# Performance work log

Measured on AMD Instinct MI355X. Metric: run time of the kernel, lower is better.

Reference implementation:

```python
import jax, jax.numpy as jnp
import numpy as np

N = 50000   # nodes
E = 800000  # edges
G = 64      # graphs in batch
EPS = 1e-5  # BatchNorm eps


def setup_inputs() -> dict:
    key = jax.random.key(0)
    ks = jax.random.split(key, 32)
    inp = {
        'x': jax.random.normal(ks[0], (N, 1), jnp.float32),
        'edge_index': jax.random.randint(ks[1], (2, E), 0, N),
        'batch': jnp.sort(jax.random.randint(ks[2], (N,), 0, G)),
    }
    dims = [(1, 64), (64, 64), (64, 64), (64, 64)]
    for i, (din, dout) in enumerate(dims, 1):
        inp[f'W{i}'] = jax.random.normal(ks[2 + i], (din, dout), jnp.float32) / np.sqrt(din)
        inp[f'b{i}'] = jnp.zeros((dout,), jnp.float32)
        inp[f'g{i}'] = jnp.ones((dout,), jnp.float32)
        inp[f'bt{i}'] = jnp.zeros((dout,), jnp.float32)
    inp['fw1'] = jax.random.normal(ks[10], (128, 64), jnp.float32) / 8.0
    inp['fb1'] = jnp.zeros((128,), jnp.float32)
    inp['fw2'] = jax.random.normal(ks[11], (10, 128), jnp.float32) / np.sqrt(128)
    inp['fb2'] = jnp.zeros((10,), jnp.float32)
    return inp


def _gcn_norm(edge_index):
    # add self-loops, symmetric normalization (PyG GCNConv default)
    loop = jnp.arange(N)
    row = jnp.concatenate([edge_index[0], loop])
    col = jnp.concatenate([edge_index[1], loop])
    deg = jax.ops.segment_sum(jnp.ones_like(col, jnp.float32), col, num_segments=N)
    dinv = jnp.where(deg > 0, deg ** -0.5, 0.0)
    norm = dinv[row] * dinv[col]
    return row, col, norm


def _gcn(x, W, b, row, col, norm):
    h = x @ W                                   # [N, dout]
    msg = h[row] * norm[:, None]                # gather + scale per edge
    agg = jax.ops.segment_sum(msg, col, num_segments=N)  # scatter-add
    return agg + b


def _bn(x, g, bt):
    m = x.mean(0)
    v = x.var(0)
    return g * (x - m) * jax.lax.rsqrt(v + EPS) + bt


def reference(x, edge_index, batch,
              W1, b1, g1, bt1, W2, b2, g2, bt2,
              W3, b3, g3, bt3, W4, b4, g4, bt4,
              fw1, fb1, fw2, fb2):
    row, col, norm = _gcn_norm(edge_index)
    x = jax.nn.relu(_bn(_gcn(x, W1, b1, row, col, norm), g1, bt1))
    x = jax.nn.relu(_bn(_gcn(x, W2, b2, row, col, norm), g2, bt2))
    x = jax.nn.relu(_bn(_gcn(x, W3, b3, row, col, norm), g3, bt3))
    x = jax.nn.relu(_bn(_gcn(x, W4, b4, row, col, norm), g4, bt4))
    # global mean pool over graphs
    cnt = jax.ops.segment_sum(jnp.ones((N,), jnp.float32), batch, num_segments=G)
    pooled = jax.ops.segment_sum(x, batch, num_segments=G) / jnp.clip(cnt, 1.0)[:, None]
    h = jax.nn.relu(pooled @ fw1.T + fb1)
    return h @ fw2.T + fb2
```

## Files before the change

### kernel.cpp

```cpp
#include <hip/hip_runtime.h>

#define NN 50000
#define NE 800000
#define NG 64
#define FD 64
#define BN_EPS 1e-5f
#define SCAN_B 256
#define SCAN_NBLK ((NN + SCAN_B - 1) / SCAN_B)
#define NBIN 98
#define BINCAP 12288
#define SCH 4096
#define SCH_NBLK ((NE + SCH - 1) / SCH)

__global__ __launch_bounds__(256) void k_binscatter(const int* __restrict__ row,
                                                    const int* __restrict__ col,
                                                    int* __restrict__ gcnt,
                                                    int* __restrict__ bins) {
    __shared__ int stage[SCH];
    __shared__ int cnt[NBIN], off[NBIN + 1], cur[NBIN], gbase[NBIN];
    int t = threadIdx.x;
    int e0 = blockIdx.x * SCH;
    int nk = NE - e0; if (nk > SCH) nk = SCH;
    if (nk <= 0) return;
    for (int b = t; b < NBIN; b += 256) cnt[b] = 0;
    __syncthreads();
    for (int k = t; k < nk; k += 256) {
        int c = col[e0 + k];
        atomicAdd(&cnt[c >> 9], 1);
    }
    __syncthreads();
    if (t == 0) {
        int run = 0;
        for (int b = 0; b < NBIN; ++b) { off[b] = run; run += cnt[b]; }
        off[NBIN] = run;
    }
    __syncthreads();
    if (t < NBIN) {
        cur[t] = off[t];
        gbase[t] = t * BINCAP + atomicAdd(&gcnt[t], cnt[t]);
    }
    __syncthreads();
    for (int k = t; k < nk; k += 256) {
        int c = col[e0 + k];
        int r = row[e0 + k];
        int b = c >> 9;
        int pos = atomicAdd(&cur[b], 1);
        stage[pos] = ((c & 511) << 16) | r;
    }
    __syncthreads();
    for (int k = t; k < nk; k += 256) {
        int lo = 0, hi = NBIN - 1;
        while (lo < hi) {
            int mid = (lo + hi + 1) >> 1;
            if (off[mid] <= k) lo = mid; else hi = mid - 1;
        }
        bins[gbase[lo] + (k - off[lo])] = stage[k];
    }
}

__global__ __launch_bounds__(256) void k_bindeg(const int* __restrict__ gcnt,
                                                const int* __restrict__ bins,
                                                int* __restrict__ deg) {
    __shared__ int ldeg[512];
    int b = blockIdx.x, t = threadIdx.x;
    for (int l = t; l < 512; l += 256) ldeg[l] = 0;
    __syncthreads();
    int nb = gcnt[b];
    const int* bp = bins + b * BINCAP;
    for (int k = t; k < nb; k += 256) atomicAdd(&ldeg[bp[k] >> 16], 1);
    __syncthreads();
    int base = b << 9;
    for (int l = t; l < 512; l += 256) {
        int i = base + l;
        if (i < NN) deg[i] = ldeg[l];
    }
}

__global__ __launch_bounds__(SCAN_B) void k_scan_blk(const int* __restrict__ deg,
                                                     int* __restrict__ cursor,
                                                     int* __restrict__ bsum,
                                                     float* __restrict__ dinv) {
    __shared__ int sh[SCAN_B];
    int b = blockIdx.x, t = threadIdx.x;
    int i = b * SCAN_B + t;
    int v = (i < NN) ? deg[i] : 0;
    if (i < NN) dinv[i] = rsqrtf((float)v + 1.0f);
    sh[t] = v;
    __syncthreads();
    for (int off = 1; off < SCAN_B; off <<= 1) {
        int u = (t >= off) ? sh[t - off] : 0;
        __syncthreads();
        sh[t] += u;
        __syncthreads();
    }
    if (i < NN) cursor[i] = sh[t] - v;
    if (t == SCAN_B - 1) bsum[b] = sh[t];
}

__global__ __launch_bounds__(SCAN_B) void k_scan_top(int* __restrict__ bsum) {
    __shared__ int sh[SCAN_B];
    int t = threadIdx.x;
    int v = (t < SCAN_NBLK) ? bsum[t] : 0;
    sh[t] = v;
    __syncthreads();
    for (int off = 1; off < SCAN_B; off <<= 1) {
        int u = (t >= off) ? sh[t - off] : 0;
        __syncthreads();
        sh[t] += u;
        __syncthreads();
    }
    if (t < SCAN_NBLK) bsum[t] = sh[t] - v;
}

__global__ __launch_bounds__(SCAN_B) void k_scan_add(int* __restrict__ cursor,
                                                     const int* __restrict__ bsum) {
    int b = blockIdx.x, t = threadIdx.x;
    int i = b * SCAN_B + t;
    if (i < NN) cursor[i] += bsum[b];
}

__global__ __launch_bounds__(256) void k_binfill(const int* __restrict__ gcnt,
                                                 const int* __restrict__ bins,
                                                 const int* __restrict__ cursor,
                                                 int* __restrict__ eidx) {
    __shared__ int lcur[512];
    int b = blockIdx.x, t = threadIdx.x;
    int base = b << 9;
    for (int l = t; l < 512; l += 256) {
        int i = base + l;
        lcur[l] = (i < NN) ? cursor[i] : 0;
    }
    __syncthreads();
    int nb = gcnt[b];
    const int* bp = bins + b * BINCAP;
    for (int k = t; k < nb; k += 256) {
        int v = bp[k];
        int pos = atomicAdd(&lcur[v >> 16], 1);
        eidx[pos] = v & 0xFFFF;
    }
}

__global__ void k_xd(const float* __restrict__ x, const float* __restrict__ dinv,
                     float* __restrict__ xd) {
    int i = blockIdx.x * blockDim.x + threadIdx.x;
    if (i < NN) xd[i] = x[i] * dinv[i];
}

__global__ void k_l1_gather(const int* __restrict__ cursor, const int* __restrict__ eidx,
                            const float* __restrict__ xd, const float* __restrict__ x,
                            const float* __restrict__ dinv, float* __restrict__ s) {
    int i = blockIdx.x * blockDim.x + threadIdx.x;
    if (i < NN) {
        int start = cursor[i];
        int end = (i < NN - 1) ? cursor[i + 1] : NE;
        float acc = 0.0f;
        for (int k = start; k < end; ++k) acc += xd[eidx[k]];
        float di = dinv[i];
        s[i] = di * (acc + di * x[i]);
    }
}

__global__ __launch_bounds__(256) void k_scalar_stats(const float* __restrict__ s,
                                                      float* __restrict__ stats) {
    __shared__ float ls[256], lq[256];
    float a = 0.f, b = 0.f;
    for (int i = blockIdx.x * blockDim.x + threadIdx.x; i < NN; i += gridDim.x * blockDim.x) {
        float v = s[i]; a += v; b += v * v;
    }
    ls[threadIdx.x] = a; lq[threadIdx.x] = b; __syncthreads();
    for (int st = 128; st > 0; st >>= 1) {
        if (threadIdx.x < st) { ls[threadIdx.x] += ls[threadIdx.x + st]; lq[threadIdx.x] += lq[threadIdx.x + st]; }
        __syncthreads();
    }
    if (threadIdx.x == 0) { atomicAdd(&stats[0], ls[0]); atomicAdd(&stats[1], lq[0]); }
}

__global__ void k_l1_coeffs(const float* __restrict__ stats, const float* __restrict__ W1,
                            const float* __restrict__ b1, const float* __restrict__ g1,
                            const float* __restrict__ bt1,
                            float* __restrict__ alpha, float* __restrict__ cshift) {
    int j = threadIdx.x;
    if (j < FD) {
        float mean = stats[0] * (1.0f / NN);
        float var  = stats[1] * (1.0f / NN) - mean * mean;
        float w = W1[j];
        float rinv = rsqrtf(var * w * w + BN_EPS);
        float a = g1[j] * w * rinv;
        alpha[j]  = a;
        cshift[j] = bt1[j] - a * mean;
    }
}

__global__ __launch_bounds__(256) void k_mm_l1(const float* __restrict__ s,
                                               const float* __restrict__ alpha,
                                               const float* __restrict__ cshift,
                                               const float* __restrict__ W,
                                               float* __restrict__ h) {
    __shared__ float Ws[64 * 64];
    __shared__ float xs[4 * 64];
    int t = threadIdx.x;
    for (int k = t; k < 64 * 64; k += 256) Ws[k] = W[k];
    int n0 = blockIdx.x * 4;
    int j = t & 63, n = t >> 6;
    int node = n0 + n;
    float sv = (node < NN) ? s[node] : 0.0f;
    xs[t] = fmaxf(alpha[j] * sv + cshift[j], 0.0f);
    __syncthreads();
    if (node < NN) {
        float acc = 0.f;
        #pragma unroll
        for (int k = 0; k < 64; ++k) acc += xs[n * 64 + k] * Ws[k * 64 + j];
        h[node * 64 + j] = acc;
    }
}

__global__ __launch_bounds__(256) void k_mm_bn(const float* __restrict__ src,
                                               const float* __restrict__ scale,
                                               const float* __restrict__ shift,
                                               const float* __restrict__ W,
                                               float* __restrict__ h) {
    __shared__ float Ws[64 * 64];
    __shared__ float xs[4 * 64];
    int t = threadIdx.x;
    for (int k = t; k < 64 * 64; k += 256) Ws[k] = W[k];
    int n0 = blockIdx.x * 4;
    int j = t & 63, n = t >> 6;
    int node = n0 + n;
    int gidx = n0 * 64 + t;
    float v = (gidx < NN * 64) ? src[gidx] : 0.0f;
    xs[t] = fmaxf(scale[j] * v + shift[j], 0.0f);
    __syncthreads();
    if (node < NN) {
        float acc = 0.f;
        #pragma unroll
        for (int k = 0; k < 64; ++k) acc += xs[n * 64 + k] * Ws[k * 64 + j];
        h[node * 64 + j] = acc;
    }
}

__global__ __launch_bounds__(256) void k_gather(const int* __restrict__ cursor,
                                                const int* __restrict__ eidx,
                                                const float* __restrict__ dinv,
                                                const float* __restrict__ h,
                                                const float* __restrict__ b,
                                                float* __restrict__ agg) {
    int node = blockIdx.x * 4 + (threadIdx.x >> 6);
    if (node >= NN) return;
    int lane = threadIdx.x & 63;
    int eslot = lane >> 4;
    int fb = (lane & 15) << 2;
    int start = cursor[node];
    int end = (node < NN - 1) ? cursor[node + 1] : NE;
    float4 acc = make_float4(0.f, 0.f, 0.f, 0.f);
    for (int e = start + eslot; e < end; e += 4) {
        int r = eidx[e];
        float dr = dinv[r];
        const float4 hv = *reinterpret_cast<const float4*>(&h[r * 64 + fb]);
        acc.x += hv.x * dr; acc.y += hv.y * dr; acc.z += hv.z * dr; acc.w += hv.w * dr;
    }
    acc.x += __shfl_xor(acc.x, 16); acc.y += __shfl_xor(acc.y, 16);
    acc.z += __shfl_xor(acc.z, 16); acc.w += __shfl_xor(acc.w, 16);
    acc.x += __shfl_xor(acc.x, 32); acc.y += __shfl_xor(acc.y, 32);
    acc.z += __shfl_xor(acc.z, 32); acc.w += __shfl_xor(acc.w, 32);
    if (lane < 16) {
        float dc = dinv[node];
        const float4 hv = *reinterpret_cast<const float4*>(&h[node * 64 + fb]);
        const float4 bv = *reinterpret_cast<const float4*>(&b[fb]);
        float4 o;
        o.x = dc * (acc.x + dc * hv.x) + bv.x;
        o.y = dc * (acc.y + dc * hv.y) + bv.y;
        o.z = dc * (acc.z + dc * hv.z) + bv.z;
        o.w = dc * (acc.w + dc * hv.w) + bv.w;
        *reinterpret_cast<float4*>(&agg[node * 64 + fb]) = o;
    }
}

__global__ __launch_bounds__(256) void k_bn_stats(const float* __restrict__ agg,
                                                  float* __restrict__ bnsum, float* __restrict__ bnsq) {
    __shared__ float ls[256], lq[256];
    int j = threadIdx.x & 63, nl = threadIdx.x >> 6;
    float a = 0.f, b = 0.f;
    for (int i = blockIdx.x * 4 + nl; i < NN; i += gridDim.x * 4) {
        float v = agg[i * 64 + j]; a += v; b += v * v;
    }
    ls[threadIdx.x] = a; lq[threadIdx.x] = b; __syncthreads();
    if (threadIdx.x < 128) { ls[threadIdx.x] += ls[threadIdx.x + 128]; lq[threadIdx.x] += lq[threadIdx.x + 128]; }
    __syncthreads();
    if (threadIdx.x < 64) {
        atomicAdd(&bnsum[j], ls[threadIdx.x] + ls[threadIdx.x + 64]);
        atomicAdd(&bnsq[j],  lq[threadIdx.x] + lq[threadIdx.x + 64]);
    }
}

__global__ void k_bn_finalize(const float* __restrict__ bnsum, const float* __restrict__ bnsq,
                              const float* __restrict__ g, const float* __restrict__ bt,
                              float* __restrict__ scale, float* __restrict__ shift) {
    int j = threadIdx.x;
    if (j < FD) {
        float mean = bnsum[j] * (1.0f / NN);
        float var  = bnsq[j] * (1.0f / NN) - mean * mean;
        float rinv = rsqrtf(var + BN_EPS);
        float sc = g[j] * rinv;
        scale[j] = sc;
        shift[j] = bt[j] - sc * mean;
    }
}

__global__ __launch_bounds__(256) void k_pool_bn(const float* __restrict__ agg,
                                                 const float* __restrict__ scale,
                                                 const float* __restrict__ shift,
                                                 const int* __restrict__ batch,
                                                 float* __restrict__ pooled,
                                                 float* __restrict__ cnt) {
    const int wpb = 4;
    int wave = blockIdx.x * wpb + (threadIdx.x >> 6);
    int lane = threadIdx.x & 63;
    const int nwaves = gridDim.x * wpb;
    int chunk = (NN + nwaves - 1) / nwaves;
    int i0 = wave * chunk;
    int i1 = i0 + chunk; if (i1 > NN) i1 = NN;
    if (i0 >= NN) return;
    float sc = scale[lane], sh = shift[lane];
    float acc = 0.0f;
    int curb = batch[i0];
    int runlen = 0;
    for (int i = i0; i < i1; ++i) {
        int b = batch[i];
        if (b != curb) {
            atomicAdd(&pooled[curb * 64 + lane], acc);
            if (lane == 0) atomicAdd(&cnt[curb], (float)runlen);
            acc = 0.0f; runlen = 0; curb = b;
        }
        acc += fmaxf(sc * agg[i * 64 + lane] + sh, 0.0f);
        ++runlen;
    }
    atomicAdd(&pooled[curb * 64 + lane], acc);
    if (lane == 0) atomicAdd(&cnt[curb], (float)runlen);
}

__global__ __launch_bounds__(128) void k_fc(const float* __restrict__ pooled, const float* __restrict__ cnt,
                                            const float* __restrict__ fw1, const float* __restrict__ fb1,
                                            const float* __restrict__ fw2, const float* __restrict__ fb2,
                                            float* __restrict__ out) {
    __shared__ float p[64], hsh[128];
    int g = blockIdx.x, t = threadIdx.x;
    if (t < 64) {
        float c = cnt[g]; c = c < 1.f ? 1.f : c;
        p[t] = pooled[g * 64 + t] / c;
    }
    __syncthreads();
    float acc = fb1[t];
    #pragma unroll 8
    for (int k = 0; k < 64; ++k) acc += p[k] * fw1[t * 64 + k];
    hsh[t] = fmaxf(acc, 0.f);
    __syncthreads();
    if (t < 10) {
        float o = fb2[t];
        #pragma unroll 8
        for (int k = 0; k < 128; ++k) o += hsh[k] * fw2[t * 128 + k];
        out[g * 10 + t] = o;
    }
}

extern "C" void kernel_launch(void* const* d_in, const int* in_sizes, int n_in,
                              void* d_out, int out_size, void* d_ws, size_t ws_size,
                              hipStream_t stream) {
    const float* x   = (const float*)d_in[0];
    const int* ei    = (const int*)d_in[1];
    const int* batch = (const int*)d_in[2];
    const float* W[5]  = {nullptr, (const float*)d_in[3],  (const float*)d_in[7],
                                   (const float*)d_in[11], (const float*)d_in[15]};
    const float* bb[5] = {nullptr, (const float*)d_in[4],  (const float*)d_in[8],
                                   (const float*)d_in[12], (const float*)d_in[16]};
    const float* gg[5] = {nullptr, (const float*)d_in[5],  (const float*)d_in[9],
                                   (const float*)d_in[13], (const float*)d_in[17]};
    const float* bt[5] = {nullptr, (const float*)d_in[6],  (const float*)d_in[10],
                                   (const float*)d_in[14], (const float*)d_in[18]};
    const float* fw1 = (const float*)d_in[19];
    const float* fb1 = (const float*)d_in[20];
    const float* fw2 = (const float*)d_in[21];
    const float* fb2 = (const float*)d_in[22];
    float* out = (float*)d_out;

    const int* row = ei;
    const int* col = ei + NE;

    float* ws = (float*)d_ws;
    int*   cursor  = (int*)ws;
    int*   degi    = (int*)(ws + 50000);
    int*   eidx    = (int*)(ws + 100000);
    float* dinv    = ws + 900000;
    float* xd      = ws + 950000;
    int*   bsum    = (int*)(ws + 1000000);
    float* s       = ws + 1001000;
    float* stats   = ws + 1051008;
    float* bnsum   = ws + 1051072;
    float* bnsq    = ws + 1051136;
    float* scale   = ws + 1051200;
    float* shift   = ws + 1051264;
    float* pooled  = ws + 1051360;
    float* cnt     = ws + 1055456;
    int*   gcnt    = (int*)(ws + 1056000);
    float* hbuf    = ws + 1100000;
    int*   bins    = (int*)(ws + 1100000);
    float* aggbuf  = ws + 4300000;

    const int B = 256;
    int gN  = (NN + B - 1) / B;

    hipMemsetAsync(gcnt, 0, NBIN * sizeof(int), stream);
    k_binscatter<<<SCH_NBLK, B, 0, stream>>>(row, col, gcnt, bins);
    k_bindeg<<<NBIN, B, 0, stream>>>(gcnt, bins, degi);
    k_scan_blk<<<SCAN_NBLK, SCAN_B, 0, stream>>>(degi, cursor, bsum, dinv);
    k_scan_top<<<1, SCAN_B, 0, stream>>>(bsum);
    k_scan_add<<<SCAN_NBLK, SCAN_B, 0, stream>>>(cursor, bsum);
    k_binfill<<<NBIN, B, 0, stream>>>(gcnt, bins, cursor, eidx);

    k_xd<<<gN, B, 0, stream>>>(x, dinv, xd);
    k_l1_gather<<<gN, B, 0, stream>>>(cursor, eidx, xd, x, dinv, s);
    hipMemsetAsync(stats, 0, 2 * sizeof(float), stream);
    k_scalar_stats<<<256, B, 0, stream>>>(s, stats);
    k_l1_coeffs<<<1, 64, 0, stream>>>(stats, W[1], bb[1], gg[1], bt[1], scale, shift);

    k_mm_l1<<<(NN + 3) / 4, B, 0, stream>>>(s, scale, shift, W[2], hbuf);
    k_gather<<<(NN + 3) / 4, B, 0, stream>>>(cursor, eidx, dinv, hbuf, bb[2], aggbuf);
    hipMemsetAsync(bnsum, 0, 128 * sizeof(float), stream);
    k_bn_stats<<<512, B, 0, stream>>>(aggbuf, bnsum, bnsq);
    k_bn_finalize<<<1, 64, 0, stream>>>(bnsum, bnsq, gg[2], bt[2], scale, shift);

    for (int L = 3; L <= 4; ++L) {
        k_mm_bn<<<(NN + 3) / 4, B, 0, stream>>>(aggbuf, scale, shift, W[L], hbuf);
        k_gather<<<(NN + 3) / 4, B, 0, stream>>>(cursor, eidx, dinv, hbuf, bb[L], aggbuf);
        hipMemsetAsync(bnsum, 0, 128 * sizeof(float), stream);
        k_bn_stats<<<512, B, 0, stream>>>(aggbuf, bnsum, bnsq);
        k_bn_finalize<<<1, 64, 0, stream>>>(bnsum, bnsq, gg[L], bt[L], scale, shift);
    }

    hipMemsetAsync(pooled, 0, (64 * 64 + 64) * sizeof(float), stream);
    k_pool_bn<<<512, B, 0, stream>>>(aggbuf, scale, shift, batch, pooled, cnt);
    k_fc<<<NG, 128, 0, stream>>>(pooled, cnt, fw1, fb1, fw2, fb2, out);
}
```

Before: 361.8 us.

## Fuse CSR build, layer-1 stats and BN finalize into neighbouring kernels

Merges degree counting with a per-bin local scan and computes dinv and xd in the same kernel. The global scan-add pass is dropped by applying bin offsets wherever the cursor is read. Layer-1 statistics are reduced inside the gather kernel, and BN scale/shift are recomputed at the start of each consumer kernel instead of in separate finalize kernels. Host memsets become in-kernel zeroing in earlier kernels. The aim is to cut kernel launches and inter-kernel gaps, at the cost of an extra bsum lookup per cursor read and redundant per-block coefficient math.

```diff
diff --git a/kernel.cpp b/kernel.cpp
--- a/kernel.cpp
+++ b/kernel.cpp
@@ -6,11 +6,11 @@
 #define FD 64
 #define BN_EPS 1e-5f
 #define SCAN_B 256
-#define SCAN_NBLK ((NN + SCAN_B - 1) / SCAN_B)
 #define NBIN 98
 #define BINCAP 12288
 #define SCH 4096
 #define SCH_NBLK ((NE + SCH - 1) / SCH)
+#define INV_NN (1.0f / NN)
 
 __global__ __launch_bounds__(256) void k_binscatter(const int* __restrict__ row,
                                                     const int* __restrict__ col,
@@ -58,10 +58,15 @@
     }
 }
 
-__global__ __launch_bounds__(256) void k_bindeg(const int* __restrict__ gcnt,
-                                                const int* __restrict__ bins,
-                                                int* __restrict__ deg) {
+__global__ __launch_bounds__(256) void k_binscan(const int* __restrict__ gcnt,
+                                                 const int* __restrict__ bins,
+                                                 const float* __restrict__ x,
+                                                 int* __restrict__ cursor,
+                                                 int* __restrict__ bsum,
+                                                 float* __restrict__ dinv,
+                                                 float* __restrict__ xd) {
     __shared__ int ldeg[512];
+    __shared__ int psc[256];
     int b = blockIdx.x, t = threadIdx.x;
     for (int l = t; l < 512; l += 256) ldeg[l] = 0;
     __syncthreads();
@@ -69,22 +74,38 @@
     const int* bp = bins + b * BINCAP;
     for (int k = t; k < nb; k += 256) atomicAdd(&ldeg[bp[k] >> 16], 1);
     __syncthreads();
+    int d0 = ldeg[2 * t], d1 = ldeg[2 * t + 1];
+    int pv = d0 + d1;
+    psc[t] = pv;
+    __syncthreads();
+    for (int off = 1; off < 256; off <<= 1) {
+        int u = (t >= off) ? psc[t - off] : 0;
+        __syncthreads();
+        psc[t] += u;
+        __syncthreads();
+    }
+    int excl = psc[t] - pv;
     int base = b << 9;
-    for (int l = t; l < 512; l += 256) {
-        int i = base + l;
-        if (i < NN) deg[i] = ldeg[l];
-    }
-}
-
-__global__ __launch_bounds__(SCAN_B) void k_scan_blk(const int* __restrict__ deg,
-                                                     int* __restrict__ cursor,
-                                                     int* __restrict__ bsum,
-                                                     float* __restrict__ dinv) {
+    int i0 = base + 2 * t, i1 = i0 + 1;
+    if (i0 < NN) {
+        cursor[i0] = excl;
+        float dv = rsqrtf((float)d0 + 1.0f);
+        dinv[i0] = dv; xd[i0] = x[i0] * dv;
+    }
+    if (i1 < NN) {
+        cursor[i1] = excl + d0;
+        float dv = rsqrtf((float)d1 + 1.0f);
+        dinv[i1] = dv; xd[i1] = x[i1] * dv;
+    }
+    if (t == 255) bsum[b] = psc[255];
+}
+
+__global__ __launch_bounds__(SCAN_B) void k_scan_top(int* __restrict__ bsum,
+                                                     float* __restrict__ stats) {
     __shared__ int sh[SCAN_B];
-    int b = blockIdx.x, t = threadIdx.x;
-    int i = b * SCAN_B + t;
-    int v = (i < NN) ? deg[i] : 0;
-    if (i < NN) dinv[i] = rsqrtf((float)v + 1.0f);
+    int t = threadIdx.x;
+    if (t < 2) stats[t] = 0.0f;
+    int v = (t < NBIN) ? bsum[t] : 0;
     sh[t] = v;
     __syncthreads();
     for (int off = 1; off < SCAN_B; off <<= 1) {
@@ -93,42 +114,21 @@
         sh[t] += u;
         __syncthreads();
     }
-    if (i < NN) cursor[i] = sh[t] - v;
-    if (t == SCAN_B - 1) bsum[b] = sh[t];
-}
-
-__global__ __launch_bounds__(SCAN_B) void k_scan_top(int* __restrict__ bsum) {
-    __shared__ int sh[SCAN_B];
-    int t = threadIdx.x;
-    int v = (t < SCAN_NBLK) ? bsum[t] : 0;
-    sh[t] = v;
-    __syncthreads();
-    for (int off = 1; off < SCAN_B; off <<= 1) {
-        int u = (t >= off) ? sh[t - off] : 0;
-        __syncthreads();
-        sh[t] += u;
-        __syncthreads();
-    }
-    if (t < SCAN_NBLK) bsum[t] = sh[t] - v;
-}
-
-__global__ __launch_bounds__(SCAN_B) void k_scan_add(int* __restrict__ cursor,
-                                                     const int* __restrict__ bsum) {
-    int b = blockIdx.x, t = threadIdx.x;
-    int i = b * SCAN_B + t;
-    if (i < NN) cursor[i] += bsum[b];
+    if (t < NBIN) bsum[t] = sh[t] - v;
 }
 
 __global__ __launch_bounds__(256) void k_binfill(const int* __restrict__ gcnt,
                                                  const int* __restrict__ bins,
                                                  const int* __restrict__ cursor,
+                                                 const int* __restrict__ bsum,
                                                  int* __restrict__ eidx) {
     __shared__ int lcur[512];
     int b = blockIdx.x, t = threadIdx.x;
     int base = b << 9;
+    int bofs = bsum[b];
     for (int l = t; l < 512; l += 256) {
         int i = base + l;
-        lcur[l] = (i < NN) ? cursor[i] : 0;
+        lcur[l] = (i < NN) ? cursor[i] + bofs : 0;
     }
     __syncthreads();
     int nb = gcnt[b];
@@ -140,71 +140,63 @@
     }
 }
 
-__global__ void k_xd(const float* __restrict__ x, const float* __restrict__ dinv,
-                     float* __restrict__ xd) {
-    int i = blockIdx.x * blockDim.x + threadIdx.x;
-    if (i < NN) xd[i] = x[i] * dinv[i];
-}
-
-__global__ void k_l1_gather(const int* __restrict__ cursor, const int* __restrict__ eidx,
-                            const float* __restrict__ xd, const float* __restrict__ x,
-                            const float* __restrict__ dinv, float* __restrict__ s) {
-    int i = blockIdx.x * blockDim.x + threadIdx.x;
+__global__ __launch_bounds__(256) void k_l1_gather(const int* __restrict__ cursor,
+                                                   const int* __restrict__ bsum,
+                                                   const int* __restrict__ eidx,
+                                                   const float* __restrict__ xd,
+                                                   const float* __restrict__ x,
+                                                   const float* __restrict__ dinv,
+                                                   float* __restrict__ s,
+                                                   float* __restrict__ stats) {
+    __shared__ float ls[256], lq[256];
+    int t = threadIdx.x;
+    int i = blockIdx.x * 256 + t;
+    float sv = 0.0f;
     if (i < NN) {
-        int start = cursor[i];
-        int end = (i < NN - 1) ? cursor[i + 1] : NE;
+        int start = cursor[i] + bsum[i >> 9];
+        int end = (i < NN - 1) ? cursor[i + 1] + bsum[(i + 1) >> 9] : NE;
         float acc = 0.0f;
         for (int k = start; k < end; ++k) acc += xd[eidx[k]];
         float di = dinv[i];
-        s[i] = di * (acc + di * x[i]);
-    }
-}
-
-__global__ __launch_bounds__(256) void k_scalar_stats(const float* __restrict__ s,
-                                                      float* __restrict__ stats) {
-    __shared__ float ls[256], lq[256];
-    float a = 0.f, b = 0.f;
-    for (int i = blockIdx.x * blockDim.x + threadIdx.x; i < NN; i += gridDim.x * blockDim.x) {
-        float v = s[i]; a += v; b += v * v;
-    }
-    ls[threadIdx.x] = a; lq[threadIdx.x] = b; __syncthreads();
+        sv = di * (acc + di * x[i]);
+        s[i] = sv;
+    }
+    ls[t] = sv; lq[t] = sv * sv;
+    __syncthreads();
     for (int st = 128; st > 0; st >>= 1) {
-        if (threadIdx.x < st) { ls[threadIdx.x] += ls[threadIdx.x + st]; lq[threadIdx.x] += lq[threadIdx.x + st]; }
+        if (t < st) { ls[t] += ls[t + st]; lq[t] += lq[t + st]; }
         __syncthreads();
     }
-    if (threadIdx.x == 0) { atomicAdd(&stats[0], ls[0]); atomicAdd(&stats[1], lq[0]); }
-}
-
-__global__ void k_l1_coeffs(const float* __restrict__ stats, const float* __restrict__ W1,
-                            const float* __restrict__ b1, const float* __restrict__ g1,
-                            const float* __restrict__ bt1,
-                            float* __restrict__ alpha, float* __restrict__ cshift) {
-    int j = threadIdx.x;
-    if (j < FD) {
-        float mean = stats[0] * (1.0f / NN);
-        float var  = stats[1] * (1.0f / NN) - mean * mean;
-        float w = W1[j];
-        float rinv = rsqrtf(var * w * w + BN_EPS);
-        float a = g1[j] * w * rinv;
-        alpha[j]  = a;
-        cshift[j] = bt1[j] - a * mean;
-    }
+    if (t == 0) { atomicAdd(&stats[0], ls[0]); atomicAdd(&stats[1], lq[0]); }
 }
 
 __global__ __launch_bounds__(256) void k_mm_l1(const float* __restrict__ s,
-                                               const float* __restrict__ alpha,
-                                               const float* __restrict__ cshift,
+                                               const float* __restrict__ stats,
+                                               const float* __restrict__ W1,
+                                               const float* __restrict__ g1,
+                                               const float* __restrict__ bt1,
                                                const float* __restrict__ W,
                                                float* __restrict__ h) {
     __shared__ float Ws[64 * 64];
     __shared__ float xs[4 * 64];
+    __shared__ float als[64], cls[64];
     int t = threadIdx.x;
     for (int k = t; k < 64 * 64; k += 256) Ws[k] = W[k];
+    if (t < 64) {
+        float mean = stats[0] * INV_NN;
+        float var  = stats[1] * INV_NN - mean * mean;
+        float w = W1[t];
+        float rinv = rsqrtf(var * w * w + BN_EPS);
+        float a = g1[t] * w * rinv;
+        als[t] = a;
+        cls[t] = bt1[t] - a * mean;
+    }
+    __syncthreads();
     int n0 = blockIdx.x * 4;
     int j = t & 63, n = t >> 6;
     int node = n0 + n;
     float sv = (node < NN) ? s[node] : 0.0f;
-    xs[t] = fmaxf(alpha[j] * sv + cshift[j], 0.0f);
+    xs[t] = fmaxf(als[j] * sv + cls[j], 0.0f);
     __syncthreads();
     if (node < NN) {
         float acc = 0.f;
@@ -215,20 +207,32 @@
 }
 
 __global__ __launch_bounds__(256) void k_mm_bn(const float* __restrict__ src,
-                                               const float* __restrict__ scale,
-                                               const float* __restrict__ shift,
+                                               const float* __restrict__ bnsum,
+                                               const float* __restrict__ bnsq,
+                                               const float* __restrict__ g,
+                                               const float* __restrict__ bt,
                                                const float* __restrict__ W,
                                                float* __restrict__ h) {
     __shared__ float Ws[64 * 64];
     __shared__ float xs[4 * 64];
+    __shared__ float scl[64], shf[64];
     int t = threadIdx.x;
     for (int k = t; k < 64 * 64; k += 256) Ws[k] = W[k];
+    if (t < 64) {
+        float mean = bnsum[t] * INV_NN;
+        float var  = bnsq[t] * INV_NN - mean * mean;
+        float rinv = rsqrtf(var + BN_EPS);
+        float sc = g[t] * rinv;
+        scl[t] = sc;
+        shf[t] = bt[t] - sc * mean;
+    }
+    __syncthreads();
     int n0 = blockIdx.x * 4;
     int j = t & 63, n = t >> 6;
     int node = n0 + n;
     int gidx = n0 * 64 + t;
     float v = (gidx < NN * 64) ? src[gidx] : 0.0f;
-    xs[t] = fmaxf(scale[j] * v + shift[j], 0.0f);
+    xs[t] = fmaxf(scl[j] * v + shf[j], 0.0f);
     __syncthreads();
     if (node < NN) {
         float acc = 0.f;
@@ -239,18 +243,26 @@
 }
 
 __global__ __launch_bounds__(256) void k_gather(const int* __restrict__ cursor,
+                                                const int* __restrict__ bsum,
                                                 const int* __restrict__ eidx,
                                                 const float* __restrict__ dinv,
                                                 const float* __restrict__ h,
                                                 const float* __restrict__ b,
-                                                float* __restrict__ agg) {
+                                                float* __restrict__ agg,
+                                                float* __restrict__ bnsumz,
+                                                float* __restrict__ bnsqz) {
+    if (blockIdx.x == 0) {
+        int t = threadIdx.x;
+        if (t < 64) bnsumz[t] = 0.0f;
+        else if (t < 128) bnsqz[t - 64] = 0.0f;
+    }
     int node = blockIdx.x * 4 + (threadIdx.x >> 6);
     if (node >= NN) return;
     int lane = threadIdx.x & 63;
     int eslot = lane >> 4;
     int fb = (lane & 15) << 2;
-    int start = cursor[node];
-    int end = (node < NN - 1) ? cursor[node + 1] : NE;
+    int start = cursor[node] + bsum[node >> 9];
+    int end = (node < NN - 1) ? cursor[node + 1] + bsum[(node + 1) >> 9] : NE;
     float4 acc = make_float4(0.f, 0.f, 0.f, 0.f);
     for (int e = start + eslot; e < end; e += 4) {
         int r = eidx[e];
@@ -276,7 +288,12 @@
 }
 
 __global__ __launch_bounds__(256) void k_bn_stats(const float* __restrict__ agg,
-                                                  float* __restrict__ bnsum, float* __restrict__ bnsq) {
+                                                  float* __restrict__ bnsum, float* __restrict__ bnsq,
+                                                  float* __restrict__ pooledz, float* __restrict__ cntz) {
+    if (pooledz != nullptr && blockIdx.x == 0) {
+        for (int k = threadIdx.x; k < 64 * 64; k += 256) pooledz[k] = 0.0f;
+        if (threadIdx.x < 64) cntz[threadIdx.x] = 0.0f;
+    }
     __shared__ float ls[256], lq[256];
     int j = threadIdx.x & 63, nl = threadIdx.x >> 6;
     float a = 0.f, b = 0.f;
@@ -292,23 +309,11 @@
     }
 }
 
-__global__ void k_bn_finalize(const float* __restrict__ bnsum, const float* __restrict__ bnsq,
-                              const float* __restrict__ g, const float* __restrict__ bt,
-                              float* __restrict__ scale, float* __restrict__ shift) {
-    int j = threadIdx.x;
-    if (j < FD) {
-        float mean = bnsum[j] * (1.0f / NN);
-        float var  = bnsq[j] * (1.0f / NN) - mean * mean;
-        float rinv = rsqrtf(var + BN_EPS);
-        float sc = g[j] * rinv;
-        scale[j] = sc;
-        shift[j] = bt[j] - sc * mean;
-    }
-}
-
 __global__ __launch_bounds__(256) void k_pool_bn(const float* __restrict__ agg,
-                                                 const float* __restrict__ scale,
-                                                 const float* __restrict__ shift,
+                                                 const float* __restrict__ bnsum,
+                                                 const float* __restrict__ bnsq,
+                                                 const float* __restrict__ g4,
+                                                 const float* __restrict__ bt4,
                                                  const int* __restrict__ batch,
                                                  float* __restrict__ pooled,
                                                  float* __restrict__ cnt) {
@@ -320,7 +325,11 @@
     int i0 = wave * chunk;
     int i1 = i0 + chunk; if (i1 > NN) i1 = NN;
     if (i0 >= NN) return;
-    float sc = scale[lane], sh = shift[lane];
+    float mean = bnsum[lane] * INV_NN;
+    float var  = bnsq[lane] * INV_NN - mean * mean;
+    float rinv = rsqrtf(var + BN_EPS);
+    float sc = g4[lane] * rinv;
+    float sh = bt4[lane] - sc * mean;
     float acc = 0.0f;
     int curb = batch[i0];
     int runlen = 0;
@@ -387,56 +396,43 @@
 
     float* ws = (float*)d_ws;
     int*   cursor  = (int*)ws;
-    int*   degi    = (int*)(ws + 50000);
-    int*   eidx    = (int*)(ws + 100000);
-    float* dinv    = ws + 900000;
-    float* xd      = ws + 950000;
-    int*   bsum    = (int*)(ws + 1000000);
-    float* s       = ws + 1001000;
-    float* stats   = ws + 1051008;
-    float* bnsum   = ws + 1051072;
-    float* bnsq    = ws + 1051136;
-    float* scale   = ws + 1051200;
-    float* shift   = ws + 1051264;
-    float* pooled  = ws + 1051360;
-    float* cnt     = ws + 1055456;
+    int*   eidx    = (int*)(ws + 50000);
+    float* dinv    = ws + 850000;
+    float* xd      = ws + 900000;
+    int*   bsum    = (int*)(ws + 950000);
+    float* s       = ws + 951000;
+    float* stats   = ws + 1001008;
+    float* bnsum   = ws + 1001072;
+    float* bnsq    = ws + 1001136;
+    float* pooled  = ws + 1001360;
+    float* cnt     = ws + 1005456;
     int*   gcnt    = (int*)(ws + 1056000);
     float* hbuf    = ws + 1100000;
     int*   bins    = (int*)(ws + 1100000);
     float* aggbuf  = ws + 4300000;
 
     const int B = 256;
-    int gN  = (NN + B - 1) / B;
+    int gN = (NN + B - 1) / B;
 
     hipMemsetAsync(gcnt, 0, NBIN * sizeof(int), stream);
     k_binscatter<<<SCH_NBLK, B, 0, stream>>>(row, col, gcnt, bins);
-    k_bindeg<<<NBIN, B, 0, stream>>>(gcnt, bins, degi);
-    k_scan_blk<<<SCAN_NBLK, SCAN_B, 0, stream>>>(degi, cursor, bsum, dinv);
-    k_scan_top<<<1, SCAN_B, 0, stream>>>(bsum);
-    k_scan_add<<<SCAN_NBLK, SCAN_B, 0, stream>>>(cursor, bsum);
-    k_binfill<<<NBIN, B, 0, stream>>>(gcnt, bins, cursor, eidx);
-
-    k_xd<<<gN, B, 0, stream>>>(x, dinv, xd);
-    k_l1_gather<<<gN, B, 0, stream>>>(cursor, eidx, xd, x, dinv, s);
-    hipMemsetAsync(stats, 0, 2 * sizeof(float), stream);
-    k_scalar_stats<<<256, B, 0, stream>>>(s, stats);
-    k_l1_coeffs<<<1, 64, 0, stream>>>(stats, W[1], bb[1], gg[1], bt[1], scale, shift);
-
-    k_mm_l1<<<(NN + 3) / 4, B, 0, stream>>>(s, scale, shift, W[2], hbuf);
-    k_gather<<<(NN + 3) / 4, B, 0, stream>>>(cursor, eidx, dinv, hbuf, bb[2], aggbuf);
-    hipMemsetAsync(bnsum, 0, 128 * sizeof(float), stream);
-    k_bn_stats<<<512, B, 0, stream>>>(aggbuf, bnsum, bnsq);
-    k_bn_finalize<<<1, 64, 0, stream>>>(bnsum, bnsq, gg[2], bt[2], scale, shift);
+    k_binscan<<<NBIN, B, 0, stream>>>(gcnt, bins, x, cursor, bsum, dinv, xd);
+    k_scan_top<<<1, SCAN_B, 0, stream>>>(bsum, stats);
+    k_binfill<<<NBIN, B, 0, stream>>>(gcnt, bins, cursor, bsum, eidx);
+
+    k_l1_gather<<<gN, B, 0, stream>>>(cursor, bsum, eidx, xd, x, dinv, s, stats);
+
+    k_mm_l1<<<(NN + 3) / 4, B, 0, stream>>>(s, stats, W[1], gg[1], bt[1], W[2], hbuf);
+    k_gather<<<(NN + 3) / 4, B, 0, stream>>>(cursor, bsum, eidx, dinv, hbuf, bb[2], aggbuf, bnsum, bnsq);
+    k_bn_stats<<<512, B, 0, stream>>>(aggbuf, bnsum, bnsq, nullptr, nullptr);
 
     for (int L = 3; L <= 4; ++L) {
-        k_mm_bn<<<(NN + 3) / 4, B, 0, stream>>>(aggbuf, scale, shift, W[L], hbuf);
-        k_gather<<<(NN + 3) / 4, B, 0, stream>>>(cursor, eidx, dinv, hbuf, bb[L], aggbuf);
-        hipMemsetAsync(bnsum, 0, 128 * sizeof(float), stream);
-        k_bn_stats<<<512, B, 0, stream>>>(aggbuf, bnsum, bnsq);
-        k_bn_finalize<<<1, 64, 0, stream>>>(bnsum, bnsq, gg[L], bt[L], scale, shift);
-    }
-
-    hipMemsetAsync(pooled, 0, (64 * 64 + 64) * sizeof(float), stream);
-    k_pool_bn<<<512, B, 0, stream>>>(aggbuf, scale, shift, batch, pooled, cnt);
+        k_mm_bn<<<(NN + 3) / 4, B, 0, stream>>>(aggbuf, bnsum, bnsq, gg[L - 1], bt[L - 1], W[L], hbuf);
+        k_gather<<<(NN + 3) / 4, B, 0, stream>>>(cursor, bsum, eidx, dinv, hbuf, bb[L], aggbuf, bnsum, bnsq);
+        k_bn_stats<<<512, B, 0, stream>>>(aggbuf, bnsum, bnsq,
+                                          (L == 4) ? pooled : nullptr, (L == 4) ? cnt : nullptr);
+    }
+
+    k_pool_bn<<<512, B, 0, stream>>>(aggbuf, bnsum, bnsq, gg[4], bt[4], batch, pooled, cnt);
     k_fc<<<NG, 128, 0, stream>>>(pooled, cnt, fw1, fb1, fw2, fb2, out);
 }
```

New measurement: 345.7 us. 1.05x faster.
